# Kernel optimization log

Hardware: AMD Instinct MI355X
Metric: run time of the kernel (lower is better)

The kernel has to match this reference:

```python
import jax, jax.numpy as jnp
import numpy as np

C, G = 128, 2000          # num_cells, total_genes
CE, GE, H = 64, 64, 256   # cell_embed_dim, gene_embed_dim, hidden_dim
F = CE + GE + 3           # FCGNN input: ctrl val + cell_embed + gene_embed + shift + num_cells


def setup_inputs() -> dict:
    key = jax.random.key(0)
    ks = jax.random.split(key, 13)
    s = 0.02
    return {
        "ctrl": jax.random.uniform(ks[0], (C, G), dtype=jnp.float32),
        "shift_vec": jax.random.normal(ks[1], (G,), dtype=jnp.float32),
        "gene_indices": jnp.arange(G, dtype=jnp.int32),
        # CellEmbedding params
        "ce_w1": jax.random.normal(ks[2], (G, H), dtype=jnp.float32) * s,
        "ce_b1": jnp.zeros((H,), dtype=jnp.float32),
        "ce_w2": jax.random.normal(ks[3], (H, CE), dtype=jnp.float32) * s,
        "ce_b2": jnp.zeros((CE,), dtype=jnp.float32),
        # gene embedding table
        "gene_table": jax.random.normal(ks[4], (G, GE), dtype=jnp.float32) * s,
        # FCGNN params
        "g_w1": jax.random.normal(ks[5], (F, H), dtype=jnp.float32) * s,
        "g_b1": jnp.zeros((H,), dtype=jnp.float32),
        "g_w2": jax.random.normal(ks[6], (2 * H, H), dtype=jnp.float32) * s,
        "g_b2": jnp.zeros((H,), dtype=jnp.float32),
        "g_w3": jax.random.normal(ks[7], (2 * H, 1), dtype=jnp.float32) * s,
        "g_b3": jnp.zeros((1,), dtype=jnp.float32),
    }


def reference(ctrl, shift_vec, gene_indices, ce_w1, ce_b1, ce_w2, ce_b2,
              gene_table, g_w1, g_b1, g_w2, g_b2, g_w3, g_b3):
    num_cells = ctrl.shape[0]
    num_genes = gene_indices.shape[0]

    # CellEmbedding: fc2(elu(fc1(ctrl)))  -> [C, CE]
    ce = jax.nn.elu(ctrl @ ce_w1 + ce_b1) @ ce_w2 + ce_b2

    ctrl_g = ctrl[:, gene_indices]           # [C, Gn]
    shift = shift_vec[gene_indices]          # [Gn]
    ge = gene_table[gene_indices]            # [Gn, GE]

    # Build [C, Gn, F] feature tensor (ctrl val, cell embed, gene embed, shift, num_cells)
    z = jnp.concatenate([
        ctrl_g[:, :, None],
        jnp.broadcast_to(ce[:, None, :], (num_cells, num_genes, ce.shape[1])),
        jnp.broadcast_to(ge[None, :, :], (num_cells, num_genes, ge.shape[1])),
        jnp.broadcast_to(shift[None, :, None], (num_cells, num_genes, 1)),
        jnp.full((num_cells, num_genes, 1), float(num_cells), dtype=ctrl.dtype),
    ], axis=2)

    # FCGNN applied per gene (vectorized over gene axis); pooling is mean over cells (axis 0)
    x = jax.nn.elu(z @ g_w1 + g_b1)                                   # [C, Gn, H]
    p = x.mean(axis=0)                                                # [Gn, H]
    x = jnp.concatenate([x, jnp.broadcast_to(p[None], x.shape)], -1) @ g_w2 + g_b2
    p = x.mean(axis=0)
    x = jax.nn.elu(jnp.concatenate([x, jnp.broadcast_to(p[None], x.shape)], -1)) @ g_w3 + g_b3
    out = x[..., 0]                                                   # [C, Gn]

    # softmax over cells (torch Softmax(dim=0) after transpose/squeeze)
    return jax.nn.softmax(out, axis=0)
```

## Files before the change

kernel.cpp:

```cpp
#include <hip/hip_runtime.h>
#include <math.h>

#define G_GENES 2000
#define C_CELLS 128
#define H_DIM   256
#define CE_DIM  64
#define LDAe    264

typedef __attribute__((ext_vector_type(8))) short short8;
typedef __attribute__((ext_vector_type(4))) float floatx4;

__device__ __forceinline__ float eluf(float x) {
    float e = __expf(x) - 1.0f;
    return x > 0.0f ? x : e;
}
__device__ __forceinline__ unsigned short f2bf(float v) {
    unsigned u = __float_as_uint(v);
    u += 0x7FFF + ((u >> 16) & 1);
    return (unsigned short)(u >> 16);
}

__global__ __launch_bounds__(256) void k1a(
    const float* __restrict__ ctrl, const float* __restrict__ ce_w1,
    float* __restrict__ hidpart)
{
    __shared__ float crow[125];
    const int c  = blockIdx.x >> 4;
    const int kc = blockIdx.x & 15;
    const int t  = threadIdx.x;

    if (t < 125) crow[t] = ctrl[(size_t)c * G_GENES + kc * 125 + t];
    __syncthreads();

    float s = 0.f;
    const float* w = ce_w1 + (size_t)(kc * 125) * H_DIM + t;
    #pragma unroll 5
    for (int k = 0; k < 125; ++k) s = fmaf(crow[k], w[(size_t)k * H_DIM], s);
    hidpart[((size_t)c * 16 + kc) * H_DIM + t] = s;
}

__global__ __launch_bounds__(256) void k1b(
    const float* __restrict__ hidpart, const float* __restrict__ ce_b1,
    const float* __restrict__ ce_w2, const float* __restrict__ ce_b2,
    const float* __restrict__ g_w1, float* __restrict__ Atc)
{
    __shared__ float hid[H_DIM];
    __shared__ float celp[4 * CE_DIM];
    __shared__ float cel[CE_DIM];
    const int c = blockIdx.x;
    const int t = threadIdx.x;

    float s = ce_b1[t];
    #pragma unroll
    for (int p = 0; p < 16; ++p) s += hidpart[((size_t)c * 16 + p) * H_DIM + t];
    hid[t] = eluf(s);
    __syncthreads();

    {
        const int e = t & 63, q4 = t >> 6;
        float cp = 0.f;
        const float* w2 = ce_w2 + (size_t)(q4 * 64) * CE_DIM + e;
        #pragma unroll 8
        for (int h = 0; h < 64; ++h) cp = fmaf(hid[q4 * 64 + h], w2[(size_t)h * CE_DIM], cp);
        celp[q4 * CE_DIM + e] = cp;
    }
    __syncthreads();
    if (t < CE_DIM)
        cel[t] = ce_b2[t] + celp[t] + celp[CE_DIM + t] + celp[2 * CE_DIM + t] + celp[3 * CE_DIM + t];
    __syncthreads();

    float a = 0.f;
    #pragma unroll 8
    for (int e = 0; e < CE_DIM; ++e) a = fmaf(cel[e], g_w1[(size_t)(1 + e) * H_DIM + t], a);
    Atc[(size_t)c * H_DIM + t] = a;
}

__global__ __launch_bounds__(256) void k_w2abt(
    const float* __restrict__ g_w2, unsigned short* __restrict__ w2abt)
{
    const int n = blockIdx.x;
    const int k = threadIdx.x;
    w2abt[(size_t)n * H_DIM + k] = f2bf(g_w2[(size_t)k * H_DIM + n]);
}

__global__ __launch_bounds__(256) void k_pqb(
    const float* __restrict__ ctrl, const float* __restrict__ shiftv,
    const int* __restrict__ gidx, const float* __restrict__ gtab,
    const float* __restrict__ g_w1, const float* __restrict__ g_b1,
    const float* __restrict__ g_w2, const float* __restrict__ g_b2,
    const float* __restrict__ Atc, float* __restrict__ Bvg,
    float* __restrict__ q_all)
{
    __shared__ float cc[C_CELLS];
    __shared__ float gt[CE_DIM];
    __shared__ float pvec[H_DIM];

    const int g = blockIdx.x;
    const int t = threadIdx.x;
    const int idx = gidx[g];

    if (t < C_CELLS) cc[t] = ctrl[(size_t)t * G_GENES + idx];
    else if (t < C_CELLS + CE_DIM) gt[t - C_CELLS] = gtab[(size_t)idx * CE_DIM + (t - C_CELLS)];
    __syncthreads();

    const float w1r0 = g_w1[t];
    float bv = g_b1[t] + 128.0f * g_w1[(size_t)130 * H_DIM + t]
             + shiftv[idx] * g_w1[(size_t)129 * H_DIM + t];
    #pragma unroll 8
    for (int e = 0; e < CE_DIM; ++e) bv = fmaf(gt[e], g_w1[(size_t)(65 + e) * H_DIM + t], bv);
    Bvg[(size_t)g * H_DIM + t] = bv;

    float s = 0.f;
    #pragma unroll 4
    for (int c = 0; c < C_CELLS; ++c)
        s += eluf(fmaf(cc[c], w1r0, Atc[(size_t)c * H_DIM + t] + bv));
    pvec[t] = s * (1.0f / 128.0f);
    __syncthreads();

    float q = g_b2[t];
    const float* w2b = g_w2 + (size_t)H_DIM * H_DIM + t;
    #pragma unroll 8
    for (int h = 0; h < H_DIM; ++h) q = fmaf(pvec[h], w2b[(size_t)h * H_DIM], q);
    q_all[(size_t)g * H_DIM + t] = q;
}

__global__ __launch_bounds__(512, 4) void k_main(
    const float* __restrict__ ctrl, const int* __restrict__ gidx,
    const float* __restrict__ g_w1, const float* __restrict__ g_w3,
    const float* __restrict__ Atc, const float* __restrict__ Bvg,
    const float* __restrict__ q_all, const unsigned short* __restrict__ w2abt,
    float* __restrict__ out)
{
    __shared__ __align__(16) unsigned short x1t[C_CELLS * LDAe];
    __shared__ float cc[C_CELLS];
    __shared__ float qv[H_DIM];
    __shared__ float w3v[H_DIM];
    __shared__ __align__(16) float Bvl[H_DIM];
    __shared__ __align__(16) float w1l[H_DIM];
    __shared__ float red2[C_CELLS * 5];
    __shared__ float wred[4];

    const int g = blockIdx.x;
    const int t = threadIdx.x;
    const int idx = gidx[g];

    if (t < C_CELLS) cc[t] = ctrl[(size_t)t * G_GENES + idx];
    if (t < H_DIM) {
        qv[t]  = q_all[(size_t)g * H_DIM + t];
        w3v[t] = g_w3[t];
    } else {
        const int u = t - H_DIM;
        Bvl[u] = Bvg[(size_t)g * H_DIM + u];
        w1l[u] = g_w1[u];
    }
    __syncthreads();

    {
        const int xc = t >> 2;
        const int xh = (t & 3) * 64;
        const float ccv = cc[xc];
        #pragma unroll
        for (int i = 0; i < 8; ++i) {
            const int h0 = xh + i * 8;
            float4 at0 = *(const float4*)(Atc + (size_t)xc * H_DIM + h0);
            float4 at1 = *(const float4*)(Atc + (size_t)xc * H_DIM + h0 + 4);
            float4 bv0 = *(const float4*)(Bvl + h0);
            float4 bv1 = *(const float4*)(Bvl + h0 + 4);
            float4 wr0 = *(const float4*)(w1l + h0);
            float4 wr1 = *(const float4*)(w1l + h0 + 4);
            float v0 = eluf(fmaf(ccv, wr0.x, at0.x + bv0.x));
            float v1 = eluf(fmaf(ccv, wr0.y, at0.y + bv0.y));
            float v2 = eluf(fmaf(ccv, wr0.z, at0.z + bv0.z));
            float v3 = eluf(fmaf(ccv, wr0.w, at0.w + bv0.w));
            float v4 = eluf(fmaf(ccv, wr1.x, at1.x + bv1.x));
            float v5 = eluf(fmaf(ccv, wr1.y, at1.y + bv1.y));
            float v6 = eluf(fmaf(ccv, wr1.z, at1.z + bv1.z));
            float v7 = eluf(fmaf(ccv, wr1.w, at1.w + bv1.w));
            uint4 pk;
            pk.x = (unsigned)f2bf(v0) | ((unsigned)f2bf(v1) << 16);
            pk.y = (unsigned)f2bf(v2) | ((unsigned)f2bf(v3) << 16);
            pk.z = (unsigned)f2bf(v4) | ((unsigned)f2bf(v5) << 16);
            pk.w = (unsigned)f2bf(v6) | ((unsigned)f2bf(v7) << 16);
            *(uint4*)&x1t[xc * LDAe + h0] = pk;
        }
    }
    __syncthreads();

    const int lane = t & 63;
    const int w    = t >> 6;
    const int quad = lane >> 4;
    const int nlo  = lane & 15;
    const int wm   = w >> 2;
    const int wn   = w & 3;

    floatx4 acc[4][4];
    #pragma unroll
    for (int mt = 0; mt < 4; ++mt)
        #pragma unroll
        for (int nt = 0; nt < 4; ++nt)
            acc[mt][nt] = (floatx4){0.f, 0.f, 0.f, 0.f};

    const unsigned short* bbase = w2abt + (size_t)(wn * 64 + nlo) * H_DIM + quad * 8;
    const unsigned short* abase = &x1t[(wm * 64 + nlo) * LDAe + quad * 8];

    for (int kt = 0; kt < 8; ++kt) {
        short8 af[4];
        #pragma unroll
        for (int mt = 0; mt < 4; ++mt)
            af[mt] = *(const short8*)(abase + mt * 16 * LDAe + kt * 32);
        #pragma unroll
        for (int nt = 0; nt < 4; ++nt) {
            short8 bf = *(const short8*)(bbase + (size_t)nt * 16 * H_DIM + kt * 32);
            #pragma unroll
            for (int mt = 0; mt < 4; ++mt)
                acc[mt][nt] = __builtin_amdgcn_mfma_f32_16x16x32_bf16(af[mt], bf, acc[mt][nt], 0, 0, 0);
        }
    }

    float qj[4], w3j[4];
    #pragma unroll
    for (int nt = 0; nt < 4; ++nt) {
        const int j = wn * 64 + nt * 16 + nlo;
        qj[nt] = qv[j];
        w3j[nt] = w3v[j];
    }
    #pragma unroll
    for (int mt = 0; mt < 4; ++mt) {
        #pragma unroll
        for (int reg = 0; reg < 4; ++reg) {
            float part = 0.f;
            #pragma unroll
            for (int nt = 0; nt < 4; ++nt)
                part = fmaf(eluf(acc[mt][nt][reg] + qj[nt]), w3j[nt], part);
            part += __shfl_xor(part, 1);
            part += __shfl_xor(part, 2);
            part += __shfl_xor(part, 4);
            part += __shfl_xor(part, 8);
            if (nlo == 0)
                red2[(wm * 64 + mt * 16 + quad * 4 + reg) * 5 + wn] = part;
        }
    }
    __syncthreads();

    float s = 0.f, e = 0.f;
    if (t < C_CELLS) {
        s = red2[t * 5 + 0] + red2[t * 5 + 1] + red2[t * 5 + 2] + red2[t * 5 + 3];
        float m = s;
        #pragma unroll
        for (int off = 1; off < 64; off <<= 1) m = fmaxf(m, __shfl_xor(m, off));
        if (lane == 0) wred[w] = m;
    }
    __syncthreads();
    if (t < C_CELLS) {
        const float m = fmaxf(wred[0], wred[1]);
        e = __expf(s - m);
        float S = e;
        #pragma unroll
        for (int off = 1; off < 64; off <<= 1) S += __shfl_xor(S, off);
        if (lane == 0) wred[2 + w] = S;
    }
    __syncthreads();
    if (t < C_CELLS) out[(size_t)t * G_GENES + g] = e / (wred[2] + wred[3]);
}

extern "C" void kernel_launch(void* const* d_in, const int* in_sizes, int n_in,
                              void* d_out, int out_size, void* d_ws, size_t ws_size,
                              hipStream_t stream) {
    const float* ctrl   = (const float*)d_in[0];
    const float* shiftv = (const float*)d_in[1];
    const int*   gidx   = (const int*)d_in[2];
    const float* ce_w1  = (const float*)d_in[3];
    const float* ce_b1  = (const float*)d_in[4];
    const float* ce_w2  = (const float*)d_in[5];
    const float* ce_b2  = (const float*)d_in[6];
    const float* gtab   = (const float*)d_in[7];
    const float* g_w1   = (const float*)d_in[8];
    const float* g_b1   = (const float*)d_in[9];
    const float* g_w2   = (const float*)d_in[10];
    const float* g_b2   = (const float*)d_in[11];
    const float* g_w3   = (const float*)d_in[12];

    char* ws = (char*)d_ws;
    float* Atc            = (float*)(ws);
    unsigned short* w2abt = (unsigned short*)(ws + 128 * 1024);
    float* Bvg            = (float*)(ws + 256 * 1024);
    float* q_all          = (float*)(ws + 256 * 1024 + (size_t)G_GENES * H_DIM * 4);
    float* hidpart        = q_all;
    float* out            = (float*)d_out;

    k1a<<<C_CELLS * 16, 256, 0, stream>>>(ctrl, ce_w1, hidpart);
    k_w2abt<<<H_DIM, 256, 0, stream>>>(g_w2, w2abt);
    k1b<<<C_CELLS, 256, 0, stream>>>(hidpart, ce_b1, ce_w2, ce_b2, g_w1, Atc);
    k_pqb<<<G_GENES, 256, 0, stream>>>(ctrl, shiftv, gidx, gtab, g_w1, g_b1, g_w2, g_b2,
                                       Atc, Bvg, q_all);
    k_main<<<G_GENES, 512, 0, stream>>>(ctrl, gidx, g_w1, g_w3, Atc, Bvg, q_all, w2abt, out);
}
```

Before: 244.8 us.

## Merge prep kernels and fold layer-1 pooling and q projection into main kernel

Four small launches (cell-embedding split-K, its reduction, the w2 transpose, and Bvg) become one heterogeneous prep kernel whose blocks are dispatched by blockIdx range. The separate per-gene pooling/q kernel is removed: k_main now sums the ELU activations while writing x1t, reduces them in shared memory, and computes the pooled q projection itself. It also prefetches the B fragments for the next k step in registers and changes the LDS row padding. This saves launches and recomputation of the layer-1 activations, but adds a serial 256x256 fp32 matvec and extra barriers to every k_main block, and the prep kernel loses k-split parallelism for the cell-embedding matmul.

After: 217.9 us. 1.12x faster.

```diff
diff --git a/kernel.cpp b/kernel.cpp
--- a/kernel.cpp
+++ b/kernel.cpp
@@ -5,7 +5,7 @@
 #define C_CELLS 128
 #define H_DIM   256
 #define CE_DIM  64
-#define LDAe    264
+#define LDAe    260
 
 typedef __attribute__((ext_vector_type(8))) short short8;
 typedef __attribute__((ext_vector_type(4))) float floatx4;
@@ -20,171 +20,117 @@
     return (unsigned short)(u >> 16);
 }
 
-__global__ __launch_bounds__(256) void k1a(
+__global__ __launch_bounds__(1024) void k_prep(
     const float* __restrict__ ctrl, const float* __restrict__ ce_w1,
-    float* __restrict__ hidpart)
+    const float* __restrict__ ce_b1, const float* __restrict__ ce_w2,
+    const float* __restrict__ ce_b2, const float* __restrict__ g_w1,
+    const float* __restrict__ g_b1, const float* __restrict__ shiftv,
+    const int* __restrict__ gidx, const float* __restrict__ gtab,
+    const float* __restrict__ g_w2,
+    float* __restrict__ Atc, unsigned short* __restrict__ w2abt,
+    float* __restrict__ Bvg)
 {
-    __shared__ float crow[125];
-    const int c  = blockIdx.x >> 4;
-    const int kc = blockIdx.x & 15;
-    const int t  = threadIdx.x;
-
-    if (t < 125) crow[t] = ctrl[(size_t)c * G_GENES + kc * 125 + t];
-    __syncthreads();
-
-    float s = 0.f;
-    const float* w = ce_w1 + (size_t)(kc * 125) * H_DIM + t;
-    #pragma unroll 5
-    for (int k = 0; k < 125; ++k) s = fmaf(crow[k], w[(size_t)k * H_DIM], s);
-    hidpart[((size_t)c * 16 + kc) * H_DIM + t] = s;
-}
-
-__global__ __launch_bounds__(256) void k1b(
-    const float* __restrict__ hidpart, const float* __restrict__ ce_b1,
-    const float* __restrict__ ce_w2, const float* __restrict__ ce_b2,
-    const float* __restrict__ g_w1, float* __restrict__ Atc)
+    const int b = blockIdx.x;
+    const int t = threadIdx.x;
+
+    if (b < C_CELLS) {
+        __shared__ float crow[G_GENES];
+        __shared__ float hidp[4][H_DIM];
+        __shared__ float hid[H_DIM];
+        __shared__ float celp[16 * CE_DIM];
+        __shared__ float cel[CE_DIM];
+        const int c = b;
+        for (int i = t; i < G_GENES; i += 1024) crow[i] = ctrl[(size_t)c * G_GENES + i];
+        __syncthreads();
+
+        {
+            const int h = t & 255, kq = t >> 8;
+            float s[10];
+            #pragma unroll
+            for (int j = 0; j < 10; ++j) s[j] = 0.f;
+            const float* w = ce_w1 + (size_t)(kq * 500) * H_DIM + h;
+            const float* cr = crow + kq * 500;
+            for (int k0 = 0; k0 < 50; ++k0) {
+                #pragma unroll
+                for (int j = 0; j < 10; ++j)
+                    s[j] = fmaf(cr[k0 * 10 + j], w[(size_t)(k0 * 10 + j) * H_DIM], s[j]);
+            }
+            float ss = 0.f;
+            #pragma unroll
+            for (int j = 0; j < 10; ++j) ss += s[j];
+            hidp[kq][h] = ss;
+        }
+        __syncthreads();
+        if (t < H_DIM)
+            hid[t] = eluf(hidp[0][t] + hidp[1][t] + hidp[2][t] + hidp[3][t] + ce_b1[t]);
+        __syncthreads();
+
+        {
+            const int e = t & 63, grp = t >> 6;
+            float cp = 0.f;
+            #pragma unroll
+            for (int hh = 0; hh < 16; ++hh)
+                cp = fmaf(hid[grp * 16 + hh], ce_w2[(size_t)(grp * 16 + hh) * CE_DIM + e], cp);
+            celp[grp * CE_DIM + e] = cp;
+        }
+        __syncthreads();
+        if (t < CE_DIM) {
+            float s = ce_b2[t];
+            #pragma unroll
+            for (int grp = 0; grp < 16; ++grp) s += celp[grp * CE_DIM + t];
+            cel[t] = s;
+        }
+        __syncthreads();
+        if (t < H_DIM) {
+            float a = 0.f;
+            #pragma unroll 8
+            for (int e = 0; e < CE_DIM; ++e) a = fmaf(cel[e], g_w1[(size_t)(1 + e) * H_DIM + t], a);
+            Atc[(size_t)c * H_DIM + t] = a;
+        }
+    } else if (b < C_CELLS + 8) {
+        const int n  = (b - C_CELLS) * 32 + (t >> 5);
+        const int k0 = (t & 31) * 8;
+        unsigned v[8];
+        #pragma unroll
+        for (int j = 0; j < 8; ++j) v[j] = f2bf(g_w2[(size_t)(k0 + j) * H_DIM + n]);
+        uint4 pk;
+        pk.x = v[0] | (v[1] << 16);
+        pk.y = v[2] | (v[3] << 16);
+        pk.z = v[4] | (v[5] << 16);
+        pk.w = v[6] | (v[7] << 16);
+        *(uint4*)&w2abt[(size_t)n * H_DIM + k0] = pk;
+    } else {
+        const int g = (b - C_CELLS - 8) * 4 + (t >> 8);
+        const int h = t & 255;
+        const int idx = gidx[g];
+        float bv = g_b1[h] + 128.0f * g_w1[(size_t)130 * H_DIM + h]
+                 + shiftv[idx] * g_w1[(size_t)129 * H_DIM + h];
+        #pragma unroll 8
+        for (int e = 0; e < CE_DIM; ++e)
+            bv = fmaf(gtab[(size_t)idx * CE_DIM + e], g_w1[(size_t)(65 + e) * H_DIM + h], bv);
+        Bvg[(size_t)g * H_DIM + h] = bv;
+    }
+}
+
+__global__ __launch_bounds__(512, 4) void k_main(
+    const float* __restrict__ ctrl, const int* __restrict__ gidx,
+    const float* __restrict__ g_w1, const float* __restrict__ g_w2,
+    const float* __restrict__ g_b2, const float* __restrict__ g_w3,
+    const float* __restrict__ Atc, const float* __restrict__ Bvg,
+    const unsigned short* __restrict__ w2abt, float* __restrict__ out)
 {
-    __shared__ float hid[H_DIM];
-    __shared__ float celp[4 * CE_DIM];
-    __shared__ float cel[CE_DIM];
-    const int c = blockIdx.x;
-    const int t = threadIdx.x;
-
-    float s = ce_b1[t];
-    #pragma unroll
-    for (int p = 0; p < 16; ++p) s += hidpart[((size_t)c * 16 + p) * H_DIM + t];
-    hid[t] = eluf(s);
-    __syncthreads();
-
-    {
-        const int e = t & 63, q4 = t >> 6;
-        float cp = 0.f;
-        const float* w2 = ce_w2 + (size_t)(q4 * 64) * CE_DIM + e;
-        #pragma unroll 8
-        for (int h = 0; h < 64; ++h) cp = fmaf(hid[q4 * 64 + h], w2[(size_t)h * CE_DIM], cp);
-        celp[q4 * CE_DIM + e] = cp;
-    }
-    __syncthreads();
-    if (t < CE_DIM)
-        cel[t] = ce_b2[t] + celp[t] + celp[CE_DIM + t] + celp[2 * CE_DIM + t] + celp[3 * CE_DIM + t];
-    __syncthreads();
-
-    float a = 0.f;
-    #pragma unroll 8
-    for (int e = 0; e < CE_DIM; ++e) a = fmaf(cel[e], g_w1[(size_t)(1 + e) * H_DIM + t], a);
-    Atc[(size_t)c * H_DIM + t] = a;
-}
-
-__global__ __launch_bounds__(256) void k_w2abt(
-    const float* __restrict__ g_w2, unsigned short* __restrict__ w2abt)
-{
-    const int n = blockIdx.x;
-    const int k = threadIdx.x;
-    w2abt[(size_t)n * H_DIM + k] = f2bf(g_w2[(size_t)k * H_DIM + n]);
-}
-
-__global__ __launch_bounds__(256) void k_pqb(
-    const float* __restrict__ ctrl, const float* __restrict__ shiftv,
-    const int* __restrict__ gidx, const float* __restrict__ gtab,
-    const float* __restrict__ g_w1, const float* __restrict__ g_b1,
-    const float* __restrict__ g_w2, const float* __restrict__ g_b2,
-    const float* __restrict__ Atc, float* __restrict__ Bvg,
-    float* __restrict__ q_all)
-{
+    __shared__ __align__(16) unsigned short x1t[C_CELLS * LDAe];
+    __shared__ __align__(16) float scratch[8 * LDAe];
+    __shared__ __align__(16) float Bvl[H_DIM];
+    __shared__ __align__(16) float w1l[H_DIM];
+    __shared__ float qv[H_DIM];
+    __shared__ float w3v[H_DIM];
     __shared__ float cc[C_CELLS];
-    __shared__ float gt[CE_DIM];
-    __shared__ float pvec[H_DIM];
+    __shared__ float wred[4];
 
     const int g = blockIdx.x;
     const int t = threadIdx.x;
     const int idx = gidx[g];
-
-    if (t < C_CELLS) cc[t] = ctrl[(size_t)t * G_GENES + idx];
-    else if (t < C_CELLS + CE_DIM) gt[t - C_CELLS] = gtab[(size_t)idx * CE_DIM + (t - C_CELLS)];
-    __syncthreads();
-
-    const float w1r0 = g_w1[t];
-    float bv = g_b1[t] + 128.0f * g_w1[(size_t)130 * H_DIM + t]
-             + shiftv[idx] * g_w1[(size_t)129 * H_DIM + t];
-    #pragma unroll 8
-    for (int e = 0; e < CE_DIM; ++e) bv = fmaf(gt[e], g_w1[(size_t)(65 + e) * H_DIM + t], bv);
-    Bvg[(size_t)g * H_DIM + t] = bv;
-
-    float s = 0.f;
-    #pragma unroll 4
-    for (int c = 0; c < C_CELLS; ++c)
-        s += eluf(fmaf(cc[c], w1r0, Atc[(size_t)c * H_DIM + t] + bv));
-    pvec[t] = s * (1.0f / 128.0f);
-    __syncthreads();
-
-    float q = g_b2[t];
-    const float* w2b = g_w2 + (size_t)H_DIM * H_DIM + t;
-    #pragma unroll 8
-    for (int h = 0; h < H_DIM; ++h) q = fmaf(pvec[h], w2b[(size_t)h * H_DIM], q);
-    q_all[(size_t)g * H_DIM + t] = q;
-}
-
-__global__ __launch_bounds__(512, 4) void k_main(
-    const float* __restrict__ ctrl, const int* __restrict__ gidx,
-    const float* __restrict__ g_w1, const float* __restrict__ g_w3,
-    const float* __restrict__ Atc, const float* __restrict__ Bvg,
-    const float* __restrict__ q_all, const unsigned short* __restrict__ w2abt,
-    float* __restrict__ out)
-{
-    __shared__ __align__(16) unsigned short x1t[C_CELLS * LDAe];
-    __shared__ float cc[C_CELLS];
-    __shared__ float qv[H_DIM];
-    __shared__ float w3v[H_DIM];
-    __shared__ __align__(16) float Bvl[H_DIM];
-    __shared__ __align__(16) float w1l[H_DIM];
-    __shared__ float red2[C_CELLS * 5];
-    __shared__ float wred[4];
-
-    const int g = blockIdx.x;
-    const int t = threadIdx.x;
-    const int idx = gidx[g];
-
-    if (t < C_CELLS) cc[t] = ctrl[(size_t)t * G_GENES + idx];
-    if (t < H_DIM) {
-        qv[t]  = q_all[(size_t)g * H_DIM + t];
-        w3v[t] = g_w3[t];
-    } else {
-        const int u = t - H_DIM;
-        Bvl[u] = Bvg[(size_t)g * H_DIM + u];
-        w1l[u] = g_w1[u];
-    }
-    __syncthreads();
-
-    {
-        const int xc = t >> 2;
-        const int xh = (t & 3) * 64;
-        const float ccv = cc[xc];
-        #pragma unroll
-        for (int i = 0; i < 8; ++i) {
-            const int h0 = xh + i * 8;
-            float4 at0 = *(const float4*)(Atc + (size_t)xc * H_DIM + h0);
-            float4 at1 = *(const float4*)(Atc + (size_t)xc * H_DIM + h0 + 4);
-            float4 bv0 = *(const float4*)(Bvl + h0);
-            float4 bv1 = *(const float4*)(Bvl + h0 + 4);
-            float4 wr0 = *(const float4*)(w1l + h0);
-            float4 wr1 = *(const float4*)(w1l + h0 + 4);
-            float v0 = eluf(fmaf(ccv, wr0.x, at0.x + bv0.x));
-            float v1 = eluf(fmaf(ccv, wr0.y, at0.y + bv0.y));
-            float v2 = eluf(fmaf(ccv, wr0.z, at0.z + bv0.z));
-            float v3 = eluf(fmaf(ccv, wr0.w, at0.w + bv0.w));
-            float v4 = eluf(fmaf(ccv, wr1.x, at1.x + bv1.x));
-            float v5 = eluf(fmaf(ccv, wr1.y, at1.y + bv1.y));
-            float v6 = eluf(fmaf(ccv, wr1.z, at1.z + bv1.z));
-            float v7 = eluf(fmaf(ccv, wr1.w, at1.w + bv1.w));
-            uint4 pk;
-            pk.x = (unsigned)f2bf(v0) | ((unsigned)f2bf(v1) << 16);
-            pk.y = (unsigned)f2bf(v2) | ((unsigned)f2bf(v3) << 16);
-            pk.z = (unsigned)f2bf(v4) | ((unsigned)f2bf(v5) << 16);
-            pk.w = (unsigned)f2bf(v6) | ((unsigned)f2bf(v7) << 16);
-            *(uint4*)&x1t[xc * LDAe + h0] = pk;
-        }
-    }
-    __syncthreads();
 
     const int lane = t & 63;
     const int w    = t >> 6;
@@ -193,6 +139,64 @@
     const int wm   = w >> 2;
     const int wn   = w & 3;
 
+    const unsigned short* bbase = w2abt + (size_t)(wn * 64 + nlo) * H_DIM + quad * 8;
+    short8 bcur[4];
+    #pragma unroll
+    for (int nt = 0; nt < 4; ++nt)
+        bcur[nt] = *(const short8*)(bbase + (size_t)nt * 16 * H_DIM);
+
+    if (t < C_CELLS) cc[t] = ctrl[(size_t)t * G_GENES + idx];
+    if (t < H_DIM) {
+        Bvl[t] = Bvg[(size_t)g * H_DIM + t];
+        w1l[t] = g_w1[t];
+        w3v[t] = g_w3[t];
+    }
+    __syncthreads();
+
+    {
+        const int ho = t & 31, cgrp = t >> 5;
+        const int h0 = ho * 8;
+        float4 wv0 = *(const float4*)(w1l + h0);
+        float4 wv1 = *(const float4*)(w1l + h0 + 4);
+        float4 bv0 = *(const float4*)(Bvl + h0);
+        float4 bv1 = *(const float4*)(Bvl + h0 + 4);
+        float s[8];
+        #pragma unroll
+        for (int j = 0; j < 8; ++j) s[j] = 0.f;
+        #pragma unroll
+        for (int i = 0; i < 8; ++i) {
+            const int c = cgrp * 8 + i;
+            const float ccv = cc[c];
+            float4 a0 = *(const float4*)(Atc + (size_t)c * H_DIM + h0);
+            float4 a1 = *(const float4*)(Atc + (size_t)c * H_DIM + h0 + 4);
+            float v0 = eluf(fmaf(ccv, wv0.x, a0.x + bv0.x));
+            float v1 = eluf(fmaf(ccv, wv0.y, a0.y + bv0.y));
+            float v2 = eluf(fmaf(ccv, wv0.z, a0.z + bv0.z));
+            float v3 = eluf(fmaf(ccv, wv0.w, a0.w + bv0.w));
+            float v4 = eluf(fmaf(ccv, wv1.x, a1.x + bv1.x));
+            float v5 = eluf(fmaf(ccv, wv1.y, a1.y + bv1.y));
+            float v6 = eluf(fmaf(ccv, wv1.z, a1.z + bv1.z));
+            float v7 = eluf(fmaf(ccv, wv1.w, a1.w + bv1.w));
+            s[0] += v0; s[1] += v1; s[2] += v2; s[3] += v3;
+            s[4] += v4; s[5] += v5; s[6] += v6; s[7] += v7;
+            uint4 pk;
+            pk.x = (unsigned)f2bf(v0) | ((unsigned)f2bf(v1) << 16);
+            pk.y = (unsigned)f2bf(v2) | ((unsigned)f2bf(v3) << 16);
+            pk.z = (unsigned)f2bf(v4) | ((unsigned)f2bf(v5) << 16);
+            pk.w = (unsigned)f2bf(v6) | ((unsigned)f2bf(v7) << 16);
+            *(uint4*)&x1t[c * LDAe + h0] = pk;
+        }
+        #pragma unroll
+        for (int j = 0; j < 8; ++j) s[j] += __shfl_xor(s[j], 32);
+        if (lane < 32) {
+            float4 p0 = {s[0], s[1], s[2], s[3]};
+            float4 p1 = {s[4], s[5], s[6], s[7]};
+            *(float4*)&scratch[w * LDAe + h0] = p0;
+            *(float4*)&scratch[w * LDAe + h0 + 4] = p1;
+        }
+    }
+    __syncthreads();
+
     floatx4 acc[4][4];
     #pragma unroll
     for (int mt = 0; mt < 4; ++mt)
@@ -200,23 +204,53 @@
         for (int nt = 0; nt < 4; ++nt)
             acc[mt][nt] = (floatx4){0.f, 0.f, 0.f, 0.f};
 
-    const unsigned short* bbase = w2abt + (size_t)(wn * 64 + nlo) * H_DIM + quad * 8;
     const unsigned short* abase = &x1t[(wm * 64 + nlo) * LDAe + quad * 8];
 
+    #pragma unroll
     for (int kt = 0; kt < 8; ++kt) {
         short8 af[4];
         #pragma unroll
         for (int mt = 0; mt < 4; ++mt)
             af[mt] = *(const short8*)(abase + mt * 16 * LDAe + kt * 32);
-        #pragma unroll
-        for (int nt = 0; nt < 4; ++nt) {
-            short8 bf = *(const short8*)(bbase + (size_t)nt * 16 * H_DIM + kt * 32);
+        short8 bnx[4];
+        if (kt < 7) {
+            #pragma unroll
+            for (int nt = 0; nt < 4; ++nt)
+                bnx[nt] = *(const short8*)(bbase + (size_t)nt * 16 * H_DIM + (kt + 1) * 32);
+        }
+        #pragma unroll
+        for (int nt = 0; nt < 4; ++nt)
             #pragma unroll
             for (int mt = 0; mt < 4; ++mt)
-                acc[mt][nt] = __builtin_amdgcn_mfma_f32_16x16x32_bf16(af[mt], bf, acc[mt][nt], 0, 0, 0);
-        }
-    }
-
+                acc[mt][nt] = __builtin_amdgcn_mfma_f32_16x16x32_bf16(af[mt], bcur[nt], acc[mt][nt], 0, 0, 0);
+        if (kt < 7) {
+            #pragma unroll
+            for (int nt = 0; nt < 4; ++nt) bcur[nt] = bnx[nt];
+        }
+    }
+
+    if (t < H_DIM) {
+        float ps = 0.f;
+        #pragma unroll
+        for (int w2 = 0; w2 < 8; ++w2) ps += scratch[w2 * LDAe + t];
+        w1l[t] = ps * (1.0f / 128.0f);
+    }
+    __syncthreads();
+
+    {
+        const int j = t & 255, hf = t >> 8;
+        float qp = 0.f;
+        const float* w2b = g_w2 + (size_t)(H_DIM + hf * 128) * H_DIM + j;
+        const float* pv = w1l + hf * 128;
+        #pragma unroll 16
+        for (int h = 0; h < 128; ++h) qp = fmaf(pv[h], w2b[(size_t)h * H_DIM], qp);
+        if (hf) Bvl[j] = qp;
+        __syncthreads();
+        if (!hf) qv[j] = qp + Bvl[j] + g_b2[j];
+    }
+    __syncthreads();
+
+    float* red2 = scratch;
     float qj[4], w3j[4];
     #pragma unroll
     for (int nt = 0; nt < 4; ++nt) {
@@ -284,14 +318,11 @@
     float* Atc            = (float*)(ws);
     unsigned short* w2abt = (unsigned short*)(ws + 128 * 1024);
     float* Bvg            = (float*)(ws + 256 * 1024);
-    float* q_all          = (float*)(ws + 256 * 1024 + (size_t)G_GENES * H_DIM * 4);
-    float* hidpart        = q_all;
     float* out            = (float*)d_out;
 
-    k1a<<<C_CELLS * 16, 256, 0, stream>>>(ctrl, ce_w1, hidpart);
-    k_w2abt<<<H_DIM, 256, 0, stream>>>(g_w2, w2abt);
-    k1b<<<C_CELLS, 256, 0, stream>>>(hidpart, ce_b1, ce_w2, ce_b2, g_w1, Atc);
-    k_pqb<<<G_GENES, 256, 0, stream>>>(ctrl, shiftv, gidx, gtab, g_w1, g_b1, g_w2, g_b2,
-                                       Atc, Bvg, q_all);
-    k_main<<<G_GENES, 512, 0, stream>>>(ctrl, gidx, g_w1, g_w3, Atc, Bvg, q_all, w2abt, out);
-}
+    k_prep<<<C_CELLS + 8 + G_GENES / 4, 1024, 0, stream>>>(
+        ctrl, ce_w1, ce_b1, ce_w2, ce_b2, g_w1, g_b1, shiftv, gidx, gtab, g_w2,
+        Atc, w2abt, Bvg);
+    k_main<<<G_GENES, 512, 0, stream>>>(ctrl, gidx, g_w1, g_w2, g_b2, g_w3,
+                                        Atc, Bvg, w2abt, out);
+}
```
